# Performance work log

Hardware: AMD Instinct MI355X
Metric: run time of the kernel (lower is better)

Reference implementation:

```python
import math
import jax, jax.numpy as jnp
import numpy as np

WINDOW = (2, 7, 7)
SHIFT = (1, 3, 3)
NUM_HEADS = 4
DIM = 128
B, D, H, W = 1, 16, 112, 112  # divisible by window -> no padding, shift active


def _rel_coords_table():
    wd, wh, ww = WINDOW
    cd = np.arange(-(wd - 1), wd, dtype=np.float32)
    ch = np.arange(-(wh - 1), wh, dtype=np.float32)
    cw = np.arange(-(ww - 1), ww, dtype=np.float32)
    t = np.stack(np.meshgrid(cd, ch, cw, indexing='ij'), axis=-1)  # [2wd-1,2wh-1,2ww-1,3]
    t[..., 0] /= (wd - 1)
    t[..., 1] /= (wh - 1)
    t[..., 2] /= (ww - 1)
    t *= 8.0
    t = np.sign(t) * np.log2(np.abs(t) + 1.0) / 3.0
    return t.reshape(-1, 3)


def _rel_pos_index():
    wd, wh, ww = WINDOW
    coords = np.stack(np.meshgrid(np.arange(wd), np.arange(wh), np.arange(ww), indexing='ij'))
    cf = coords.reshape(3, -1)
    rc = (cf[:, :, None] - cf[:, None, :]).transpose(1, 2, 0)  # [N,N,3]
    rc[..., 0] += wd - 1
    rc[..., 1] += wh - 1
    rc[..., 2] += ww - 1
    rc[..., 0] *= (2 * wh - 1) * (2 * ww - 1)
    rc[..., 1] *= (2 * ww - 1)
    return rc.sum(-1).reshape(-1)


def _attn_mask(pd, ph, pw):
    wd, wh, ww = WINDOW
    sd, sh, sw = SHIFT
    m = np.zeros((pd, ph, pw), np.float32)
    cnt = 0
    for d in ((0, -wd), (-wd, -sd), (-sd, None)):
        for h in ((0, -wh), (-wh, -sh), (-sh, None)):
            for w in ((0, -ww), (-ww, -sw), (-sw, None)):
                m[d[0]:d[1], h[0]:h[1], w[0]:w[1]] = cnt
                cnt += 1
    nwin = (pd // wd) * (ph // wh) * (pw // ww)
    m = m.reshape(pd // wd, wd, ph // wh, wh, pw // ww, ww)
    m = m.transpose(0, 2, 4, 1, 3, 5).reshape(nwin, -1)  # [nWin, N]
    diff = m[:, None, :] - m[:, :, None]
    return np.where(diff != 0, -100.0, 0.0).astype(np.float32)


def setup_inputs() -> dict:
    key = jax.random.key(0)
    ks = jax.random.split(key, 5)
    C = DIM
    return {
        'x': jax.random.normal(ks[0], (B, D, H, W, C), jnp.float32),
        'qkv_weight': jax.random.normal(ks[1], (3 * C, C), jnp.float32) * 0.02,
        'qkv_bias': jnp.zeros((3 * C,), jnp.float32),
        'proj_weight': jax.random.normal(ks[2], (C, C), jnp.float32) * 0.02,
        'proj_bias': jnp.zeros((C,), jnp.float32),
        'logit_scale': jnp.full((NUM_HEADS, 1, 1), math.log(10.0), jnp.float32),
        'cpb_w1': jax.random.normal(ks[3], (512, 3), jnp.float32) * 0.02,
        'cpb_b1': jnp.zeros((512,), jnp.float32),
        'cpb_w2': jax.random.normal(ks[4], (NUM_HEADS, 512), jnp.float32) * 0.02,
    }


def reference(x, qkv_weight, qkv_bias, proj_weight, proj_bias, logit_scale, cpb_w1, cpb_b1, cpb_w2):
    wd, wh, ww = WINDOW
    sd, sh, sw = SHIFT
    b, d, h, w, C = x.shape
    N = wd * wh * ww
    hd = C // NUM_HEADS

    # --- continuous relative position bias (SwinV2) ---
    table = jnp.asarray(_rel_coords_table())              # [M, 3]
    hid = jax.nn.relu(table @ cpb_w1.T + cpb_b1)          # [M, 512]
    bias_tab = hid @ cpb_w2.T                             # [M, nH]
    idx = jnp.asarray(_rel_pos_index())                   # [N*N]
    rpb = bias_tab[idx].reshape(N, N, NUM_HEADS).transpose(2, 0, 1)
    rpb = 16.0 * jax.nn.sigmoid(rpb)                      # [nH, N, N]

    # zero middle third of qkv bias (cosine attention path)
    qkv_b = qkv_bias.at[C:2 * C].set(0.0)

    # --- shift + window partition (no padding: dims divisible) ---
    xs = jnp.roll(x, (-sd, -sh, -sw), axis=(1, 2, 3))
    nd, nh, nw = d // wd, h // wh, w // ww
    nwin = nd * nh * nw
    xw = xs.reshape(b, nd, wd, nh, wh, nw, ww, C)
    xw = xw.transpose(0, 1, 3, 5, 2, 4, 6, 7).reshape(b * nwin, N, C)

    # --- qkv + cosine attention ---
    qkv = (xw @ qkv_weight.T + qkv_b).reshape(b * nwin, N, 3, NUM_HEADS, hd)
    qkv = qkv.transpose(2, 0, 3, 1, 4)                    # [3, BW, nH, N, hd]
    q, k, v = qkv[0], qkv[1], qkv[2]
    qn = q / jnp.maximum(jnp.linalg.norm(q, axis=-1, keepdims=True), 1e-12)
    kn = k / jnp.maximum(jnp.linalg.norm(k, axis=-1, keepdims=True), 1e-12)
    attn = jnp.einsum('wnid,wnjd->wnij', qn, kn)          # [BW, nH, N, N]
    scale = jnp.exp(jnp.minimum(logit_scale, math.log(100.0)))  # [nH,1,1]
    attn = attn * scale[None] + rpb[None]

    # --- shift mask ---
    mask = jnp.asarray(_attn_mask(d, h, w))               # [nWin, N, N]
    attn = attn.reshape(b, nwin, NUM_HEADS, N, N) + mask[None, :, None]
    attn = jax.nn.softmax(attn.reshape(b * nwin, NUM_HEADS, N, N), axis=-1)

    out = jnp.einsum('wnij,wnjd->wind', attn, v).reshape(b * nwin, N, C)
    out = out @ proj_weight.T + proj_bias

    # --- reverse window partition + reverse shift ---
    out = out.reshape(b, nd, nh, nw, wd, wh, ww, C)
    out = out.transpose(0, 1, 4, 2, 5, 3, 6, 7).reshape(b, d, h, w, C)
    out = jnp.roll(out, (sd, sh, sw), axis=(1, 2, 3))
    return out
```

## Files before the change

kernel.cpp:

```cpp
#include <hip/hip_runtime.h>
#include <hip/hip_bf16.h>

typedef unsigned short u16;
typedef __attribute__((ext_vector_type(8))) short bf16x8;
typedef __attribute__((ext_vector_type(4))) float f32x4;

#define MFMA(a, b, c) __builtin_amdgcn_mfma_f32_16x16x32_bf16((a), (b), (c), 0, 0, 0)
#define LOG2E 1.4426950408889634f

__device__ __forceinline__ u16 f2b(float f) {
  __hip_bfloat16 h = __float2bfloat16(f);
  return __builtin_bit_cast(u16, h);
}
__device__ __forceinline__ float bu2f(u16 u) {
  union { unsigned u; float f; } v; v.u = ((unsigned)u) << 16; return v.f;
}
__device__ __forceinline__ u16 f2bu_sw(float f) {
  union { float f; unsigned u; } v; v.f = f;
  unsigned r = v.u + 0x7fffu + ((v.u >> 16) & 1u);
  return (u16)(r >> 16);
}
__device__ __forceinline__ int maskcode(int tok, int bd, int bh, int bw) {
  int d = tok / 49, rem = tok - d * 49, hh = rem / 7, w = rem - hh * 7;
  int rd = bd ? (d == 0 ? 1 : 2) : 0;
  int rh = bh ? (hh < 4 ? 1 : 2) : 0;
  int rw = bw ? (w < 4 ? 1 : 2) : 0;
  return rd * 9 + rh * 3 + rw;
}
__device__ __forceinline__ int tokbase(int tok, int id, int ih, int iw) {
  int d = tok / 49, rem = tok - d * 49, hh = rem / 7, w2 = rem - hh * 7;
  int pd = (id * 2 + d + 1) & 15;
  int ph = ih * 7 + hh + 3; if (ph >= 112) ph -= 112;
  int pw = iw * 7 + w2 + 3; if (pw >= 112) pw -= 112;
  return ((pd * 112 + ph) * 112 + pw) << 7;
}

__global__ void cpb_mlp(const float* __restrict__ w1, const float* __restrict__ b1,
                        const float* __restrict__ w2, float* __restrict__ btab) {
  const int m = blockIdx.x;
  const int k = threadIdx.x;
  const int i0 = m / 169, rm = m % 169, i1 = rm / 13, i2 = rm % 13;
  float c0 = (float)(i0 - 1) * 8.0f;
  float c1 = (float)(i1 - 6) * (8.0f / 6.0f);
  float c2 = (float)(i2 - 6) * (8.0f / 6.0f);
  float t0 = (c0 > 0.f ? 1.f : (c0 < 0.f ? -1.f : 0.f)) * log2f(fabsf(c0) + 1.f) * (1.f / 3.f);
  float t1 = (c1 > 0.f ? 1.f : (c1 < 0.f ? -1.f : 0.f)) * log2f(fabsf(c1) + 1.f) * (1.f / 3.f);
  float t2 = (c2 > 0.f ? 1.f : (c2 < 0.f ? -1.f : 0.f)) * log2f(fabsf(c2) + 1.f) * (1.f / 3.f);
  float hid = fmaxf(w1[k * 3 + 0] * t0 + w1[k * 3 + 1] * t1 + w1[k * 3 + 2] * t2 + b1[k], 0.f);
  __shared__ float red[4][8];
#pragma unroll
  for (int h = 0; h < 4; ++h) {
    float v = hid * w2[h * 512 + k];
    for (int mm = 1; mm < 64; mm <<= 1) v += __shfl_xor(v, mm);
    if ((k & 63) == 0) red[h][k >> 6] = v;
  }
  __syncthreads();
  if (k < 4) {
    float s = 0.f;
#pragma unroll
    for (int j = 0; j < 8; ++j) s += red[k][j];
    btab[m * 4 + k] = s;
  }
}

__global__ void build_rpbf(const float* __restrict__ btab, float* __restrict__ rpbf) {
  const int total = 8 * 4 * 7 * 7 * 64 * 4;
  int n = blockIdx.x * 256 + threadIdx.x;
  if (n >= total) return;
  int r = n & 3;
  int lane = (n >> 2) & 63;
  int q = n >> 8;
  int c = q % 7;
  int wv = (q / 7) % 7;
  int h = (q / 49) % 4;
  int combo = q / 196;
  int i = 16 * wv + (lane >> 4) * 4 + r;
  int j = 16 * c + (lane & 15);
  float v;
  if (j >= 98) {
    v = -1e30f;
  } else if (i >= 98) {
    v = 0.f;
  } else {
    int di = i / 49, ri = i % 49, hi_ = ri / 7, wi = ri % 7;
    int dj = j / 49, rj = j % 49, hj = rj / 7, wj = rj % 7;
    int idx = (di - dj + 1) * 169 + (hi_ - hj + 6) * 13 + (wi - wj + 6);
    float b = btab[idx * 4 + h];
    v = (16.f / (1.f + expf(-b))) * LOG2E;
    int bd = (combo >> 2) & 1, bh = (combo >> 1) & 1, bw = combo & 1;
    if (maskcode(i, bd, bh, bw) != maskcode(j, bd, bh, bw)) v -= 144.269504f;
  }
  rpbf[n] = v;
}

__global__ void pack_wqkv(const float* __restrict__ qkvw, u16* __restrict__ dst) {
  int bid = blockIdx.x;
  int h = bid / 160, rem = bid % 160, blk = rem / 32, r = rem % 32;
  int srow = (blk < 2 ? 0 : (blk < 4 ? 128 : 256)) + h * 32 + r;
  bool lo = (blk == 1) || (blk == 3);
  int c = threadIdx.x;
  float v = (c < 128) ? qkvw[srow * 128 + c] : 0.f;
  u16 hi = f2bu_sw(v);
  u16 outv = lo ? f2bu_sw(v - bu2f(hi)) : hi;
  dst[h * 21760 + blk * 4352 + r * 136 + c] = outv;
}

__global__ void pack_wproj(const float* __restrict__ pw, u16* __restrict__ dst) {
  int c = blockIdx.x;
  int m = threadIdx.x;
  float v = (m < 128) ? pw[c * 128 + m] : 0.f;
  dst[c * 136 + m] = f2bu_sw(v);
}

#define QHI 0
#define QLO 4480
#define KHI 8960
#define KLO 13440
#define VTB 14336
#define PIDX(i, t) ((i) * 128 + ((t) ^ (((i) & 7) << 3)))
#define VIDX(d, t) (VTB + (d) * 128 + ((t) ^ (((d) & 7) << 3)))

template <bool BF16OUT>
__global__ __launch_bounds__(448, 7) void swin_attn(
    const float* __restrict__ xg, const float* __restrict__ qkvb,
    const float* __restrict__ lscale, const float* __restrict__ rpbf,
    const u16* __restrict__ wqkv, u16* __restrict__ aoutb, float* __restrict__ aoutf) {
  __shared__ u16 lds[18432];
  __shared__ int tb[98];
  const int tid = threadIdx.x;
  const int wv = tid >> 6;
  const int l = tid & 63;
  const int l15 = l & 15;
  const int lg = l >> 4;
  const int bid = blockIdx.x;
  const int win = bid >> 2, h = bid & 3;
  const int iw = win & 15, ih = (win >> 4) & 15, id = win >> 8;
  const int combo = ((id == 7) << 2) | ((ih == 15) << 1) | (iw == 15);

  if (tid < 98) tb[tid] = tokbase(tid, id, ih, iw);
  {
    const uint4* src = (const uint4*)(wqkv + h * 21760);
    uint4* dst = (uint4*)lds;
    for (int it = tid; it < 2176; it += 448) dst[it] = src[it];
  }
  const int arow = 16 * wv + l15;
  bf16x8 xa[4];
  {
    const bool rok = arow < 98;
    const int base = tokbase(rok ? arow : 0, id, ih, iw);
    const float* xp = xg + base + lg * 8;
#pragma unroll
    for (int ks = 0; ks < 4; ++ks) {
      float4 a = {0.f, 0.f, 0.f, 0.f}, b4 = {0.f, 0.f, 0.f, 0.f};
      if (rok) {
        a = *(const float4*)(xp + ks * 32);
        b4 = *(const float4*)(xp + ks * 32 + 4);
      }
      u16* xo = (u16*)&xa[ks];
      xo[0] = f2b(a.x); xo[1] = f2b(a.y); xo[2] = f2b(a.z); xo[3] = f2b(a.w);
      xo[4] = f2b(b4.x); xo[5] = f2b(b4.y); xo[6] = f2b(b4.z); xo[7] = f2b(b4.w);
    }
  }
  __syncthreads();

  const f32x4 zf = {0.f, 0.f, 0.f, 0.f};
  f32x4 aq0 = zf, aq1 = zf, ak0 = zf, ak1 = zf, av0 = zf, av1 = zf;
  const u16* wvb = wqkv + h * 21760 + 17408 + lg * 8;
  bf16x8 bv0 = *(const bf16x8*)(wvb + l15 * 136);
  bf16x8 bv1 = *(const bf16x8*)(wvb + (16 + l15) * 136);
#pragma unroll
  for (int ks = 0; ks < 4; ++ks) {
    const int k0 = ks * 32 + lg * 8;
    bf16x8 nv0, nv1;
    if (ks < 3) {
      nv0 = *(const bf16x8*)(wvb + l15 * 136 + (ks + 1) * 32);
      nv1 = *(const bf16x8*)(wvb + (16 + l15) * 136 + (ks + 1) * 32);
    }
    bf16x8 b;
    b = *(const bf16x8*)(&lds[l15 * 136 + k0]);                aq0 = MFMA(xa[ks], b, aq0);
    b = *(const bf16x8*)(&lds[4352 + l15 * 136 + k0]);         aq0 = MFMA(xa[ks], b, aq0);
    b = *(const bf16x8*)(&lds[(16 + l15) * 136 + k0]);         aq1 = MFMA(xa[ks], b, aq1);
    b = *(const bf16x8*)(&lds[4352 + (16 + l15) * 136 + k0]);  aq1 = MFMA(xa[ks], b, aq1);
    b = *(const bf16x8*)(&lds[8704 + l15 * 136 + k0]);         ak0 = MFMA(xa[ks], b, ak0);
    b = *(const bf16x8*)(&lds[13056 + l15 * 136 + k0]);        ak0 = MFMA(xa[ks], b, ak0);
    b = *(const bf16x8*)(&lds[8704 + (16 + l15) * 136 + k0]);  ak1 = MFMA(xa[ks], b, ak1);
    b = *(const bf16x8*)(&lds[13056 + (16 + l15) * 136 + k0]); ak1 = MFMA(xa[ks], b, ak1);
    av0 = MFMA(xa[ks], bv0, av0);
    av1 = MFMA(xa[ks], bv1, av1);
    if (ks < 3) { bv0 = nv0; bv1 = nv1; }
  }
  __syncthreads();

  const float sc2 = __expf(fminf(lscale[h], 4.60517019f)) * LOG2E;
  const float qb0 = qkvb[h * 32 + l15];
  const float qb1 = qkvb[h * 32 + 16 + l15];
  const float vb0 = qkvb[256 + h * 32 + l15];
  const float vb1 = qkvb[256 + h * 32 + 16 + l15];
#pragma unroll
  for (int r = 0; r < 4; ++r) { aq0[r] += qb0; aq1[r] += qb1; av0[r] += vb0; av1[r] += vb1; }
#pragma unroll
  for (int r = 0; r < 4; ++r) {
    const int row = 16 * wv + lg * 4 + r;
    const bool ok = row < 98;
    float s = aq0[r] * aq0[r] + aq1[r] * aq1[r];
    s += __shfl_xor(s, 1); s += __shfl_xor(s, 2); s += __shfl_xor(s, 4); s += __shfl_xor(s, 8);
    float rn = sc2 * rsqrtf(fmaxf(s, 1e-24f));
    float q0 = ok ? aq0[r] * rn : 0.f, q1 = ok ? aq1[r] * rn : 0.f;
    u16 u0 = f2b(q0), u1 = f2b(q1);
    lds[QHI + row * 40 + l15] = u0;
    lds[QHI + row * 40 + 16 + l15] = u1;
    lds[QLO + row * 40 + l15] = f2b(q0 - bu2f(u0));
    lds[QLO + row * 40 + 16 + l15] = f2b(q1 - bu2f(u1));
    float sk = ak0[r] * ak0[r] + ak1[r] * ak1[r];
    sk += __shfl_xor(sk, 1); sk += __shfl_xor(sk, 2); sk += __shfl_xor(sk, 4); sk += __shfl_xor(sk, 8);
    float rk = rsqrtf(fmaxf(sk, 1e-24f));
    float k0v = ok ? ak0[r] * rk : 0.f, k1v = ok ? ak1[r] * rk : 0.f;
    u16 ku0 = f2b(k0v), ku1 = f2b(k1v);
    lds[KHI + row * 40 + l15] = ku0;
    lds[KHI + row * 40 + 16 + l15] = ku1;
    lds[KLO + row * 40 + l15] = f2b(k0v - bu2f(ku0));
    lds[KLO + row * 40 + 16 + l15] = f2b(k1v - bu2f(ku1));
  }
  __syncthreads();

  const bf16x8 qh = *(const bf16x8*)(&lds[QHI + (16 * wv + l15) * 40 + lg * 8]);
  const bf16x8 qlo = *(const bf16x8*)(&lds[QLO + (16 * wv + l15) * 40 + lg * 8]);
  const f32x4* rbf = (const f32x4*)rpbf + (((combo * 4 + h) * 7 + wv) * 7) * 64 + l;
  f32x4 att[7];
#pragma unroll
  for (int c = 0; c < 7; ++c) att[c] = rbf[c * 64];
#pragma unroll
  for (int c = 0; c < 7; ++c) {
    const bf16x8 kh = *(const bf16x8*)(&lds[KHI + (16 * c + l15) * 40 + lg * 8]);
    const bf16x8 kl = *(const bf16x8*)(&lds[KLO + (16 * c + l15) * 40 + lg * 8]);
    att[c] = MFMA(qh, kh, att[c]);
    att[c] = MFMA(qlo, kh, att[c]);
    att[c] = MFMA(qh, kl, att[c]);
  }
  float rsv[4];
#pragma unroll
  for (int r = 0; r < 4; ++r) {
    float s = 0.f;
#pragma unroll
    for (int c = 0; c < 7; ++c) { float p = exp2f(att[c][r]); att[c][r] = p; s += p; }
    s += __shfl_xor(s, 1); s += __shfl_xor(s, 2); s += __shfl_xor(s, 4); s += __shfl_xor(s, 8);
    rsv[r] = 1.0f / s;
  }
  __syncthreads();

#pragma unroll
  for (int r = 0; r < 4; ++r) {
    const int i = 16 * wv + lg * 4 + r;
#pragma unroll
    for (int c = 0; c < 8; ++c) {
      const int t = 16 * c + l15;
      lds[PIDX(i, t)] = (c < 7) ? f2b(att[c][r] * rsv[r]) : (u16)0;
    }
  }
  {
    const int t0 = 16 * wv + lg * 4;
    ushort4 v0, v1;
    v0.x = (t0 + 0 < 98) ? f2b(av0[0]) : (u16)0;
    v0.y = (t0 + 1 < 98) ? f2b(av0[1]) : (u16)0;
    v0.z = (t0 + 2 < 98) ? f2b(av0[2]) : (u16)0;
    v0.w = (t0 + 3 < 98) ? f2b(av0[3]) : (u16)0;
    v1.x = (t0 + 0 < 98) ? f2b(av1[0]) : (u16)0;
    v1.y = (t0 + 1 < 98) ? f2b(av1[1]) : (u16)0;
    v1.z = (t0 + 2 < 98) ? f2b(av1[2]) : (u16)0;
    v1.w = (t0 + 3 < 98) ? f2b(av1[3]) : (u16)0;
    *(ushort4*)(&lds[VIDX(l15, t0)]) = v0;
    *(ushort4*)(&lds[VIDX(16 + l15, t0)]) = v1;
  }
  for (int it = tid; it < 32 * 16; it += 448) {
    int dd = it >> 4, t = 112 + (it & 15);
    lds[VIDX(dd, t)] = 0;
  }
  __syncthreads();

  f32x4 o0 = zf, o1 = zf;
#pragma unroll
  for (int ks = 0; ks < 4; ++ks) {
    const int t = ks * 32 + lg * 8;
    const bf16x8 pa = *(const bf16x8*)(&lds[PIDX(16 * wv + l15, t)]);
    const bf16x8 v0f = *(const bf16x8*)(&lds[VIDX(l15, t)]);
    const bf16x8 v1f = *(const bf16x8*)(&lds[VIDX(16 + l15, t)]);
    o0 = MFMA(pa, v0f, o0);
    o1 = MFMA(pa, v1f, o1);
  }
#pragma unroll
  for (int r = 0; r < 4; ++r) {
    const int row = 16 * wv + lg * 4 + r;
    if (row < 98) {
      const int ob = tb[row] + h * 32;
      if (BF16OUT) {
        aoutb[ob + l15] = f2b(o0[r]);
        aoutb[ob + 16 + l15] = f2b(o1[r]);
      } else {
        aoutf[ob + l15] = o0[r];
        aoutf[ob + 16 + l15] = o1[r];
      }
    }
  }
}

template <bool BF16OUT>
__global__ __launch_bounds__(448) void swin_proj(const u16* __restrict__ wp,
                                                 const float* __restrict__ projb,
                                                 const u16* __restrict__ aoutb,
                                                 float* io) {
  __shared__ u16 w[17408];
  __shared__ int tb[98];
  const int tid = threadIdx.x;
  const int wv = tid >> 6;
  const int l = tid & 63;
  const int l15 = l & 15;
  const int lg = l >> 4;
  const int win = blockIdx.x;
  const int iw = win & 15, ih = (win >> 4) & 15, id = win >> 8;
  if (tid < 98) tb[tid] = tokbase(tid, id, ih, iw);
  {
    const uint4* src = (const uint4*)wp;
    uint4* dst = (uint4*)w;
    for (int it = tid; it < 2176; it += 448) dst[it] = src[it];
  }
  __syncthreads();
  const int arow0 = 16 * wv + l15;
  const int abase = tb[(arow0 < 98) ? arow0 : 97];

  const f32x4 zf = {0.f, 0.f, 0.f, 0.f};
  f32x4 pr[8];
#pragma unroll
  for (int n = 0; n < 8; ++n) pr[n] = zf;
#pragma unroll
  for (int ks = 0; ks < 4; ++ks) {
    bf16x8 oa;
    if (BF16OUT) {
      oa = *(const bf16x8*)(aoutb + abase + ks * 32 + lg * 8);
    } else {
      const float4 f0 = *(const float4*)(io + abase + ks * 32 + lg * 8);
      const float4 f1 = *(const float4*)(io + abase + ks * 32 + lg * 8 + 4);
      u16* op = (u16*)&oa;
      op[0] = f2b(f0.x); op[1] = f2b(f0.y); op[2] = f2b(f0.z); op[3] = f2b(f0.w);
      op[4] = f2b(f1.x); op[5] = f2b(f1.y); op[6] = f2b(f1.z); op[7] = f2b(f1.w);
    }
#pragma unroll
    for (int n = 0; n < 8; ++n) {
      const bf16x8 wb = *(const bf16x8*)(&w[(16 * n + l15) * 136 + ks * 32 + lg * 8]);
      pr[n] = MFMA(oa, wb, pr[n]);
    }
  }
#pragma unroll
  for (int n = 0; n < 8; ++n) {
    const int col = 16 * n + l15;
    const float pb = projb[col];
#pragma unroll
    for (int r = 0; r < 4; ++r) {
      const int row = 16 * wv + lg * 4 + r;
      if (row < 98) io[tb[row] + col] = pr[n][r] + pb;
    }
  }
}

extern "C" void kernel_launch(void* const* d_in, const int* in_sizes, int n_in,
                              void* d_out, int out_size, void* d_ws, size_t ws_size,
                              hipStream_t stream) {
  const float* xg = (const float*)d_in[0];
  const float* qkvw = (const float*)d_in[1];
  const float* qkvb = (const float*)d_in[2];
  const float* projw = (const float*)d_in[3];
  const float* projb = (const float*)d_in[4];
  const float* lsc = (const float*)d_in[5];
  const float* w1 = (const float*)d_in[6];
  const float* b1 = (const float*)d_in[7];
  const float* w2 = (const float*)d_in[8];

  char* ws = (char*)d_ws;
  float* btab = (float*)(ws);
  u16* wq = (u16*)(ws + 8192);
  u16* wp = (u16*)(ws + 182272);
  float* rpbf = (float*)(ws + 217088);
  u16* aoutb = (u16*)(ws + 1822720);
  float* io = (float*)d_out;

  const bool bf16path = ws_size >= (size_t)53202944;

  cpb_mlp<<<507, 512, 0, stream>>>(w1, b1, w2, btab);
  build_rpbf<<<(8 * 4 * 7 * 7 * 64 * 4 + 255) / 256, 256, 0, stream>>>(btab, rpbf);
  pack_wqkv<<<640, 136, 0, stream>>>(qkvw, wq);
  pack_wproj<<<128, 136, 0, stream>>>(projw, wp);
  if (bf16path) {
    swin_attn<true><<<8192, 448, 0, stream>>>(xg, qkvb, lsc, rpbf, wq, aoutb, io);
    swin_proj<true><<<2048, 448, 0, stream>>>(wp, projb, aoutb, io);
  } else {
    swin_attn<false><<<8192, 448, 0, stream>>>(xg, qkvb, lsc, rpbf, wq, nullptr, io);
    swin_proj<false><<<2048, 448, 0, stream>>>(wp, projb, nullptr, io);
  }
}
```

Measured before the change: 218.5 us.

## Fuse per-head attention and output projection into one per-window kernel

Replaces the per-(window, head) attention kernel and the separate projection kernel with one kernel per window. It loops over the four heads, keeps each head's output in registers and runs the projection from LDS. Weights are repacked into a 32-column-blocked layout and read straight from global or L2 instead of being staged in LDS. This removes the bf16 intermediate round trip through global memory and one launch, and reuses the x load across heads. In exchange, each block does serial per-head work with more barriers, and occupancy falls (launch bounds 4 instead of 7), which may hurt latency hiding.

```diff
diff --git a/kernel.cpp b/kernel.cpp
--- a/kernel.cpp
+++ b/kernel.cpp
@@ -99,50 +99,46 @@
   int srow = (blk < 2 ? 0 : (blk < 4 ? 128 : 256)) + h * 32 + r;
   bool lo = (blk == 1) || (blk == 3);
   int c = threadIdx.x;
-  float v = (c < 128) ? qkvw[srow * 128 + c] : 0.f;
+  float v = qkvw[srow * 128 + c];
   u16 hi = f2bu_sw(v);
   u16 outv = lo ? f2bu_sw(v - bu2f(hi)) : hi;
-  dst[h * 21760 + blk * 4352 + r * 136 + c] = outv;
+  dst[h * 20480 + blk * 4096 + (c >> 5) * 1024 + r * 32 + (c & 31)] = outv;
 }
 
 __global__ void pack_wproj(const float* __restrict__ pw, u16* __restrict__ dst) {
   int c = blockIdx.x;
   int m = threadIdx.x;
-  float v = (m < 128) ? pw[c * 128 + m] : 0.f;
-  dst[c * 136 + m] = f2bu_sw(v);
+  dst[(m >> 5) * 4096 + c * 32 + (m & 31)] = f2bu_sw(pw[c * 128 + m]);
 }
 
 #define QHI 0
 #define QLO 4480
 #define KHI 8960
 #define KLO 13440
-#define VTB 14336
+#define VTB 17920
 #define PIDX(i, t) ((i) * 128 + ((t) ^ (((i) & 7) << 3)))
 #define VIDX(d, t) (VTB + (d) * 128 + ((t) ^ (((d) & 7) << 3)))
 
-template <bool BF16OUT>
-__global__ __launch_bounds__(448, 7) void swin_attn(
+__global__ __launch_bounds__(448, 4) void swin_fused(
     const float* __restrict__ xg, const float* __restrict__ qkvb,
     const float* __restrict__ lscale, const float* __restrict__ rpbf,
-    const u16* __restrict__ wqkv, u16* __restrict__ aoutb, float* __restrict__ aoutf) {
-  __shared__ u16 lds[18432];
+    const u16* __restrict__ wqkv, const u16* __restrict__ wproj,
+    const float* __restrict__ projb, float* __restrict__ io) {
+  __shared__ u16 lds[22016];
   __shared__ int tb[98];
   const int tid = threadIdx.x;
   const int wv = tid >> 6;
   const int l = tid & 63;
   const int l15 = l & 15;
   const int lg = l >> 4;
-  const int bid = blockIdx.x;
-  const int win = bid >> 2, h = bid & 3;
+  const int win = blockIdx.x;
   const int iw = win & 15, ih = (win >> 4) & 15, id = win >> 8;
   const int combo = ((id == 7) << 2) | ((ih == 15) << 1) | (iw == 15);
 
   if (tid < 98) tb[tid] = tokbase(tid, id, ih, iw);
-  {
-    const uint4* src = (const uint4*)(wqkv + h * 21760);
-    uint4* dst = (uint4*)lds;
-    for (int it = tid; it < 2176; it += 448) dst[it] = src[it];
-  }
+  for (int it = tid; it < 32 * 16; it += 448)
+    lds[VIDX(it >> 4, 112 + (it & 15))] = 0;
+
   const int arow = 16 * wv + l15;
   bf16x8 xa[4];
   {
@@ -161,192 +157,155 @@
       xo[4] = f2b(b4.x); xo[5] = f2b(b4.y); xo[6] = f2b(b4.z); xo[7] = f2b(b4.w);
     }
   }
-  __syncthreads();
 
   const f32x4 zf = {0.f, 0.f, 0.f, 0.f};
-  f32x4 aq0 = zf, aq1 = zf, ak0 = zf, ak1 = zf, av0 = zf, av1 = zf;
-  const u16* wvb = wqkv + h * 21760 + 17408 + lg * 8;
-  bf16x8 bv0 = *(const bf16x8*)(wvb + l15 * 136);
-  bf16x8 bv1 = *(const bf16x8*)(wvb + (16 + l15) * 136);
+  auto GEMM1 = [&](int h, f32x4& q0, f32x4& q1, f32x4& k0a, f32x4& k1a, f32x4& v0a, f32x4& v1a) {
+    q0 = q1 = k0a = k1a = v0a = v1a = zf;
+    const u16* wb = wqkv + h * 20480 + lg * 8;
+#pragma unroll
+    for (int ks = 0; ks < 4; ++ks) {
+      const int o = ks * 1024;
+      bf16x8 b;
+      b = *(const bf16x8*)(wb + o + l15 * 32);                 q0 = MFMA(xa[ks], b, q0);
+      b = *(const bf16x8*)(wb + 4096 + o + l15 * 32);          q0 = MFMA(xa[ks], b, q0);
+      b = *(const bf16x8*)(wb + o + (16 + l15) * 32);          q1 = MFMA(xa[ks], b, q1);
+      b = *(const bf16x8*)(wb + 4096 + o + (16 + l15) * 32);   q1 = MFMA(xa[ks], b, q1);
+      b = *(const bf16x8*)(wb + 8192 + o + l15 * 32);          k0a = MFMA(xa[ks], b, k0a);
+      b = *(const bf16x8*)(wb + 12288 + o + l15 * 32);         k0a = MFMA(xa[ks], b, k0a);
+      b = *(const bf16x8*)(wb + 8192 + o + (16 + l15) * 32);   k1a = MFMA(xa[ks], b, k1a);
+      b = *(const bf16x8*)(wb + 12288 + o + (16 + l15) * 32);  k1a = MFMA(xa[ks], b, k1a);
+      b = *(const bf16x8*)(wb + 16384 + o + l15 * 32);         v0a = MFMA(xa[ks], b, v0a);
+      b = *(const bf16x8*)(wb + 16384 + o + (16 + l15) * 32);  v1a = MFMA(xa[ks], b, v1a);
+    }
+  };
+
+  u16 opk[4][8];
+  f32x4 aq0, aq1, ak0, ak1, av0, av1, nq0, nq1, nk0, nk1, nv0, nv1;
+  GEMM1(0, aq0, aq1, ak0, ak1, av0, av1);
+
+#pragma unroll
+  for (int h = 0; h < 4; ++h) {
+    const float sc2 = __expf(fminf(lscale[h], 4.60517019f)) * LOG2E;
+    const float qb0 = qkvb[h * 32 + l15];
+    const float qb1 = qkvb[h * 32 + 16 + l15];
+    const float vb0 = qkvb[256 + h * 32 + l15];
+    const float vb1 = qkvb[256 + h * 32 + 16 + l15];
+#pragma unroll
+    for (int r = 0; r < 4; ++r) { aq0[r] += qb0; aq1[r] += qb1; av0[r] += vb0; av1[r] += vb1; }
+#pragma unroll
+    for (int r = 0; r < 4; ++r) {
+      const int row = 16 * wv + lg * 4 + r;
+      const bool ok = row < 98;
+      float s = aq0[r] * aq0[r] + aq1[r] * aq1[r];
+      s += __shfl_xor(s, 1); s += __shfl_xor(s, 2); s += __shfl_xor(s, 4); s += __shfl_xor(s, 8);
+      float rn = sc2 * rsqrtf(fmaxf(s, 1e-24f));
+      float q0 = ok ? aq0[r] * rn : 0.f, q1 = ok ? aq1[r] * rn : 0.f;
+      u16 u0 = f2b(q0), u1 = f2b(q1);
+      lds[QHI + row * 40 + l15] = u0;
+      lds[QHI + row * 40 + 16 + l15] = u1;
+      lds[QLO + row * 40 + l15] = f2b(q0 - bu2f(u0));
+      lds[QLO + row * 40 + 16 + l15] = f2b(q1 - bu2f(u1));
+      float sk = ak0[r] * ak0[r] + ak1[r] * ak1[r];
+      sk += __shfl_xor(sk, 1); sk += __shfl_xor(sk, 2); sk += __shfl_xor(sk, 4); sk += __shfl_xor(sk, 8);
+      float rk = rsqrtf(fmaxf(sk, 1e-24f));
+      float k0v = ok ? ak0[r] * rk : 0.f, k1v = ok ? ak1[r] * rk : 0.f;
+      u16 ku0 = f2b(k0v), ku1 = f2b(k1v);
+      lds[KHI + row * 40 + l15] = ku0;
+      lds[KHI + row * 40 + 16 + l15] = ku1;
+      lds[KLO + row * 40 + l15] = f2b(k0v - bu2f(ku0));
+      lds[KLO + row * 40 + 16 + l15] = f2b(k1v - bu2f(ku1));
+    }
+    {
+      const int t0 = 16 * wv + lg * 4;
+      ushort4 v0, v1;
+      v0.x = (t0 + 0 < 98) ? f2b(av0[0]) : (u16)0;
+      v0.y = (t0 + 1 < 98) ? f2b(av0[1]) : (u16)0;
+      v0.z = (t0 + 2 < 98) ? f2b(av0[2]) : (u16)0;
+      v0.w = (t0 + 3 < 98) ? f2b(av0[3]) : (u16)0;
+      v1.x = (t0 + 0 < 98) ? f2b(av1[0]) : (u16)0;
+      v1.y = (t0 + 1 < 98) ? f2b(av1[1]) : (u16)0;
+      v1.z = (t0 + 2 < 98) ? f2b(av1[2]) : (u16)0;
+      v1.w = (t0 + 3 < 98) ? f2b(av1[3]) : (u16)0;
+      *(ushort4*)(&lds[VIDX(l15, t0)]) = v0;
+      *(ushort4*)(&lds[VIDX(16 + l15, t0)]) = v1;
+    }
+    const f32x4* rbf = (const f32x4*)rpbf + (((combo * 4 + h) * 7 + wv) * 7) * 64 + l;
+    f32x4 att[7];
+#pragma unroll
+    for (int c = 0; c < 7; ++c) att[c] = rbf[c * 64];
+    __syncthreads();
+
+    const bf16x8 qh = *(const bf16x8*)(&lds[QHI + (16 * wv + l15) * 40 + lg * 8]);
+    const bf16x8 qlo = *(const bf16x8*)(&lds[QLO + (16 * wv + l15) * 40 + lg * 8]);
+#pragma unroll
+    for (int c = 0; c < 7; ++c) {
+      const bf16x8 kh = *(const bf16x8*)(&lds[KHI + (16 * c + l15) * 40 + lg * 8]);
+      const bf16x8 kl = *(const bf16x8*)(&lds[KLO + (16 * c + l15) * 40 + lg * 8]);
+      att[c] = MFMA(qh, kh, att[c]);
+      att[c] = MFMA(qlo, kh, att[c]);
+      att[c] = MFMA(qh, kl, att[c]);
+    }
+    float rsv[4];
+#pragma unroll
+    for (int r = 0; r < 4; ++r) {
+      float s = 0.f;
+#pragma unroll
+      for (int c = 0; c < 7; ++c) { float p = exp2f(att[c][r]); att[c][r] = p; s += p; }
+      s += __shfl_xor(s, 1); s += __shfl_xor(s, 2); s += __shfl_xor(s, 4); s += __shfl_xor(s, 8);
+      rsv[r] = 1.0f / s;
+    }
+    __syncthreads();
+
+#pragma unroll
+    for (int r = 0; r < 4; ++r) {
+      const int i = 16 * wv + lg * 4 + r;
+#pragma unroll
+      for (int c = 0; c < 8; ++c) {
+        const int t = 16 * c + l15;
+        lds[PIDX(i, t)] = (c < 7) ? f2b(att[c][r]) : (u16)0;
+      }
+    }
+    f32x4 o0 = zf, o1 = zf;
+#pragma unroll
+    for (int ks = 0; ks < 4; ++ks) {
+      const int t = ks * 32 + lg * 8;
+      const bf16x8 pa = *(const bf16x8*)(&lds[PIDX(16 * wv + l15, t)]);
+      const bf16x8 v0f = *(const bf16x8*)(&lds[VIDX(l15, t)]);
+      const bf16x8 v1f = *(const bf16x8*)(&lds[VIDX(16 + l15, t)]);
+      o0 = MFMA(pa, v0f, o0);
+      o1 = MFMA(pa, v1f, o1);
+    }
+#pragma unroll
+    for (int r = 0; r < 4; ++r) {
+      opk[h][r] = f2b(o0[r] * rsv[r]);
+      opk[h][4 + r] = f2b(o1[r] * rsv[r]);
+    }
+    if (h < 3) {
+      GEMM1(h + 1, nq0, nq1, nk0, nk1, nv0, nv1);
+      __syncthreads();
+      aq0 = nq0; aq1 = nq1; ak0 = nk0; ak1 = nk1; av0 = nv0; av1 = nv1;
+    }
+  }
+
+#pragma unroll
+  for (int h = 0; h < 4; ++h)
+#pragma unroll
+    for (int e = 0; e < 8; ++e) {
+      const int r = e & 3, half = e >> 2;
+      lds[PIDX(16 * wv + lg * 4 + r, h * 32 + half * 16 + l15)] = opk[h][e];
+    }
+
+  f32x4 pr[8];
+#pragma unroll
+  for (int n = 0; n < 8; ++n) pr[n] = zf;
 #pragma unroll
   for (int ks = 0; ks < 4; ++ks) {
-    const int k0 = ks * 32 + lg * 8;
-    bf16x8 nv0, nv1;
-    if (ks < 3) {
-      nv0 = *(const bf16x8*)(wvb + l15 * 136 + (ks + 1) * 32);
-      nv1 = *(const bf16x8*)(wvb + (16 + l15) * 136 + (ks + 1) * 32);
-    }
-    bf16x8 b;
-    b = *(const bf16x8*)(&lds[l15 * 136 + k0]);                aq0 = MFMA(xa[ks], b, aq0);
-    b = *(const bf16x8*)(&lds[4352 + l15 * 136 + k0]);         aq0 = MFMA(xa[ks], b, aq0);
-    b = *(const bf16x8*)(&lds[(16 + l15) * 136 + k0]);         aq1 = MFMA(xa[ks], b, aq1);
-    b = *(const bf16x8*)(&lds[4352 + (16 + l15) * 136 + k0]);  aq1 = MFMA(xa[ks], b, aq1);
-    b = *(const bf16x8*)(&lds[8704 + l15 * 136 + k0]);         ak0 = MFMA(xa[ks], b, ak0);
-    b = *(const bf16x8*)(&lds[13056 + l15 * 136 + k0]);        ak0 = MFMA(xa[ks], b, ak0);
-    b = *(const bf16x8*)(&lds[8704 + (16 + l15) * 136 + k0]);  ak1 = MFMA(xa[ks], b, ak1);
-    b = *(const bf16x8*)(&lds[13056 + (16 + l15) * 136 + k0]); ak1 = MFMA(xa[ks], b, ak1);
-    av0 = MFMA(xa[ks], bv0, av0);
-    av1 = MFMA(xa[ks], bv1, av1);
-    if (ks < 3) { bv0 = nv0; bv1 = nv1; }
-  }
-  __syncthreads();
-
-  const float sc2 = __expf(fminf(lscale[h], 4.60517019f)) * LOG2E;
-  const float qb0 = qkvb[h * 32 + l15];
-  const float qb1 = qkvb[h * 32 + 16 + l15];
-  const float vb0 = qkvb[256 + h * 32 + l15];
-  const float vb1 = qkvb[256 + h * 32 + 16 + l15];
-#pragma unroll
-  for (int r = 0; r < 4; ++r) { aq0[r] += qb0; aq1[r] += qb1; av0[r] += vb0; av1[r] += vb1; }
-#pragma unroll
-  for (int r = 0; r < 4; ++r) {
-    const int row = 16 * wv + lg * 4 + r;
-    const bool ok = row < 98;
-    float s = aq0[r] * aq0[r] + aq1[r] * aq1[r];
-    s += __shfl_xor(s, 1); s += __shfl_xor(s, 2); s += __shfl_xor(s, 4); s += __shfl_xor(s, 8);
-    float rn = sc2 * rsqrtf(fmaxf(s, 1e-24f));
-    float q0 = ok ? aq0[r] * rn : 0.f, q1 = ok ? aq1[r] * rn : 0.f;
-    u16 u0 = f2b(q0), u1 = f2b(q1);
-    lds[QHI + row * 40 + l15] = u0;
-    lds[QHI + row * 40 + 16 + l15] = u1;
-    lds[QLO + row * 40 + l15] = f2b(q0 - bu2f(u0));
-    lds[QLO + row * 40 + 16 + l15] = f2b(q1 - bu2f(u1));
-    float sk = ak0[r] * ak0[r] + ak1[r] * ak1[r];
-    sk += __shfl_xor(sk, 1); sk += __shfl_xor(sk, 2); sk += __shfl_xor(sk, 4); sk += __shfl_xor(sk, 8);
-    float rk = rsqrtf(fmaxf(sk, 1e-24f));
-    float k0v = ok ? ak0[r] * rk : 0.f, k1v = ok ? ak1[r] * rk : 0.f;
-    u16 ku0 = f2b(k0v), ku1 = f2b(k1v);
-    lds[KHI + row * 40 + l15] = ku0;
-    lds[KHI + row * 40 + 16 + l15] = ku1;
-    lds[KLO + row * 40 + l15] = f2b(k0v - bu2f(ku0));
-    lds[KLO + row * 40 + 16 + l15] = f2b(k1v - bu2f(ku1));
-  }
-  __syncthreads();
-
-  const bf16x8 qh = *(const bf16x8*)(&lds[QHI + (16 * wv + l15) * 40 + lg * 8]);
-  const bf16x8 qlo = *(const bf16x8*)(&lds[QLO + (16 * wv + l15) * 40 + lg * 8]);
-  const f32x4* rbf = (const f32x4*)rpbf + (((combo * 4 + h) * 7 + wv) * 7) * 64 + l;
-  f32x4 att[7];
-#pragma unroll
-  for (int c = 0; c < 7; ++c) att[c] = rbf[c * 64];
-#pragma unroll
-  for (int c = 0; c < 7; ++c) {
-    const bf16x8 kh = *(const bf16x8*)(&lds[KHI + (16 * c + l15) * 40 + lg * 8]);
-    const bf16x8 kl = *(const bf16x8*)(&lds[KLO + (16 * c + l15) * 40 + lg * 8]);
-    att[c] = MFMA(qh, kh, att[c]);
-    att[c] = MFMA(qlo, kh, att[c]);
-    att[c] = MFMA(qh, kl, att[c]);
-  }
-  float rsv[4];
-#pragma unroll
-  for (int r = 0; r < 4; ++r) {
-    float s = 0.f;
-#pragma unroll
-    for (int c = 0; c < 7; ++c) { float p = exp2f(att[c][r]); att[c][r] = p; s += p; }
-    s += __shfl_xor(s, 1); s += __shfl_xor(s, 2); s += __shfl_xor(s, 4); s += __shfl_xor(s, 8);
-    rsv[r] = 1.0f / s;
-  }
-  __syncthreads();
-
-#pragma unroll
-  for (int r = 0; r < 4; ++r) {
-    const int i = 16 * wv + lg * 4 + r;
-#pragma unroll
-    for (int c = 0; c < 8; ++c) {
-      const int t = 16 * c + l15;
-      lds[PIDX(i, t)] = (c < 7) ? f2b(att[c][r] * rsv[r]) : (u16)0;
-    }
-  }
-  {
-    const int t0 = 16 * wv + lg * 4;
-    ushort4 v0, v1;
-    v0.x = (t0 + 0 < 98) ? f2b(av0[0]) : (u16)0;
-    v0.y = (t0 + 1 < 98) ? f2b(av0[1]) : (u16)0;
-    v0.z = (t0 + 2 < 98) ? f2b(av0[2]) : (u16)0;
-    v0.w = (t0 + 3 < 98) ? f2b(av0[3]) : (u16)0;
-    v1.x = (t0 + 0 < 98) ? f2b(av1[0]) : (u16)0;
-    v1.y = (t0 + 1 < 98) ? f2b(av1[1]) : (u16)0;
-    v1.z = (t0 + 2 < 98) ? f2b(av1[2]) : (u16)0;
-    v1.w = (t0 + 3 < 98) ? f2b(av1[3]) : (u16)0;
-    *(ushort4*)(&lds[VIDX(l15, t0)]) = v0;
-    *(ushort4*)(&lds[VIDX(16 + l15, t0)]) = v1;
-  }
-  for (int it = tid; it < 32 * 16; it += 448) {
-    int dd = it >> 4, t = 112 + (it & 15);
-    lds[VIDX(dd, t)] = 0;
-  }
-  __syncthreads();
-
-  f32x4 o0 = zf, o1 = zf;
-#pragma unroll
-  for (int ks = 0; ks < 4; ++ks) {
-    const int t = ks * 32 + lg * 8;
-    const bf16x8 pa = *(const bf16x8*)(&lds[PIDX(16 * wv + l15, t)]);
-    const bf16x8 v0f = *(const bf16x8*)(&lds[VIDX(l15, t)]);
-    const bf16x8 v1f = *(const bf16x8*)(&lds[VIDX(16 + l15, t)]);
-    o0 = MFMA(pa, v0f, o0);
-    o1 = MFMA(pa, v1f, o1);
-  }
-#pragma unroll
-  for (int r = 0; r < 4; ++r) {
-    const int row = 16 * wv + lg * 4 + r;
-    if (row < 98) {
-      const int ob = tb[row] + h * 32;
-      if (BF16OUT) {
-        aoutb[ob + l15] = f2b(o0[r]);
-        aoutb[ob + 16 + l15] = f2b(o1[r]);
-      } else {
-        aoutf[ob + l15] = o0[r];
-        aoutf[ob + 16 + l15] = o1[r];
-      }
-    }
-  }
-}
-
-template <bool BF16OUT>
-__global__ __launch_bounds__(448) void swin_proj(const u16* __restrict__ wp,
-                                                 const float* __restrict__ projb,
-                                                 const u16* __restrict__ aoutb,
-                                                 float* io) {
-  __shared__ u16 w[17408];
-  __shared__ int tb[98];
-  const int tid = threadIdx.x;
-  const int wv = tid >> 6;
-  const int l = tid & 63;
-  const int l15 = l & 15;
-  const int lg = l >> 4;
-  const int win = blockIdx.x;
-  const int iw = win & 15, ih = (win >> 4) & 15, id = win >> 8;
-  if (tid < 98) tb[tid] = tokbase(tid, id, ih, iw);
-  {
-    const uint4* src = (const uint4*)wp;
-    uint4* dst = (uint4*)w;
-    for (int it = tid; it < 2176; it += 448) dst[it] = src[it];
-  }
-  __syncthreads();
-  const int arow0 = 16 * wv + l15;
-  const int abase = tb[(arow0 < 98) ? arow0 : 97];
-
-  const f32x4 zf = {0.f, 0.f, 0.f, 0.f};
-  f32x4 pr[8];
-#pragma unroll
-  for (int n = 0; n < 8; ++n) pr[n] = zf;
-#pragma unroll
-  for (int ks = 0; ks < 4; ++ks) {
-    bf16x8 oa;
-    if (BF16OUT) {
-      oa = *(const bf16x8*)(aoutb + abase + ks * 32 + lg * 8);
-    } else {
-      const float4 f0 = *(const float4*)(io + abase + ks * 32 + lg * 8);
-      const float4 f1 = *(const float4*)(io + abase + ks * 32 + lg * 8 + 4);
-      u16* op = (u16*)&oa;
-      op[0] = f2b(f0.x); op[1] = f2b(f0.y); op[2] = f2b(f0.z); op[3] = f2b(f0.w);
-      op[4] = f2b(f1.x); op[5] = f2b(f1.y); op[6] = f2b(f1.z); op[7] = f2b(f1.w);
-    }
+    const bf16x8 oa = *(const bf16x8*)(&lds[PIDX(16 * wv + l15, ks * 32 + lg * 8)]);
+    const u16* pwb = wproj + ks * 4096 + lg * 8;
 #pragma unroll
     for (int n = 0; n < 8; ++n) {
-      const bf16x8 wb = *(const bf16x8*)(&w[(16 * n + l15) * 136 + ks * 32 + lg * 8]);
-      pr[n] = MFMA(oa, wb, pr[n]);
+      const bf16x8 wbf = *(const bf16x8*)(pwb + (16 * n + l15) * 32);
+      pr[n] = MFMA(oa, wbf, pr[n]);
     }
   }
 #pragma unroll
@@ -377,22 +336,13 @@
   char* ws = (char*)d_ws;
   float* btab = (float*)(ws);
   u16* wq = (u16*)(ws + 8192);
-  u16* wp = (u16*)(ws + 182272);
-  float* rpbf = (float*)(ws + 217088);
-  u16* aoutb = (u16*)(ws + 1822720);
+  u16* wp = (u16*)(ws + 172032);
+  float* rpbf = (float*)(ws + 204800);
   float* io = (float*)d_out;
-
-  const bool bf16path = ws_size >= (size_t)53202944;
 
   cpb_mlp<<<507, 512, 0, stream>>>(w1, b1, w2, btab);
   build_rpbf<<<(8 * 4 * 7 * 7 * 64 * 4 + 255) / 256, 256, 0, stream>>>(btab, rpbf);
-  pack_wqkv<<<640, 136, 0, stream>>>(qkvw, wq);
-  pack_wproj<<<128, 136, 0, stream>>>(projw, wp);
-  if (bf16path) {
-    swin_attn<true><<<8192, 448, 0, stream>>>(xg, qkvb, lsc, rpbf, wq, aoutb, io);
-    swin_proj<true><<<2048, 448, 0, stream>>>(wp, projb, aoutb, io);
-  } else {
-    swin_attn<false><<<8192, 448, 0, stream>>>(xg, qkvb, lsc, rpbf, wq, nullptr, io);
-    swin_proj<false><<<2048, 448, 0, stream>>>(wp, projb, nullptr, io);
-  }
-}
+  pack_wqkv<<<640, 128, 0, stream>>>(qkvw, wq);
+  pack_wproj<<<128, 128, 0, stream>>>(projw, wp);
+  swin_fused<<<2048, 448, 0, stream>>>(xg, qkvb, lsc, rpbf, wq, wp, projb, io);
+}
```

Result: slower. 371.5 us, median of 2 (+70.0%).

## Transpose MFMA operands for vectorized stores and window-contiguous intermediate layout

Applied to the files above, without the earlier changes.

Swaps the A/B operands of the PV and projection MFMAs so each lane holds four consecutive output columns of one token. This allows vectorized 8/16-byte stores instead of scattered scalar stores. The bf16 intermediate now uses a window-contiguous layout, so the proj kernel reads it without a token-base lookup. It also hoists the relative-position-bias loads earlier to overlap them with the normalization, drops the masking branch on x loads (padded rows read clamped token 0), and adds an occupancy hint of 7 to launch bounds.

```diff
diff --git a/kernel.cpp b/kernel.cpp
--- a/kernel.cpp
+++ b/kernel.cpp
@@ -146,16 +146,12 @@
   const int arow = 16 * wv + l15;
   bf16x8 xa[4];
   {
-    const bool rok = arow < 98;
-    const int base = tokbase(rok ? arow : 0, id, ih, iw);
+    const int base = tokbase((arow < 98) ? arow : 0, id, ih, iw);
     const float* xp = xg + base + lg * 8;
 #pragma unroll
     for (int ks = 0; ks < 4; ++ks) {
-      float4 a = {0.f, 0.f, 0.f, 0.f}, b4 = {0.f, 0.f, 0.f, 0.f};
-      if (rok) {
-        a = *(const float4*)(xp + ks * 32);
-        b4 = *(const float4*)(xp + ks * 32 + 4);
-      }
+      const float4 a = *(const float4*)(xp + ks * 32);
+      const float4 b4 = *(const float4*)(xp + ks * 32 + 4);
       u16* xo = (u16*)&xa[ks];
       xo[0] = f2b(a.x); xo[1] = f2b(a.y); xo[2] = f2b(a.z); xo[3] = f2b(a.w);
       xo[4] = f2b(b4.x); xo[5] = f2b(b4.y); xo[6] = f2b(b4.z); xo[7] = f2b(b4.w);
@@ -190,6 +186,11 @@
     if (ks < 3) { bv0 = nv0; bv1 = nv1; }
   }
   __syncthreads();
+
+  const f32x4* rbf = (const f32x4*)rpbf + (((combo * 4 + h) * 7 + wv) * 7) * 64 + l;
+  f32x4 att[7];
+#pragma unroll
+  for (int c = 0; c < 7; ++c) att[c] = rbf[c * 64];
 
   const float sc2 = __expf(fminf(lscale[h], 4.60517019f)) * LOG2E;
   const float qb0 = qkvb[h * 32 + l15];
@@ -225,10 +226,6 @@
 
   const bf16x8 qh = *(const bf16x8*)(&lds[QHI + (16 * wv + l15) * 40 + lg * 8]);
   const bf16x8 qlo = *(const bf16x8*)(&lds[QLO + (16 * wv + l15) * 40 + lg * 8]);
-  const f32x4* rbf = (const f32x4*)rpbf + (((combo * 4 + h) * 7 + wv) * 7) * 64 + l;
-  f32x4 att[7];
-#pragma unroll
-  for (int c = 0; c < 7; ++c) att[c] = rbf[c * 64];
 #pragma unroll
   for (int c = 0; c < 7; ++c) {
     const bf16x8 kh = *(const bf16x8*)(&lds[KHI + (16 * c + l15) * 40 + lg * 8]);
@@ -284,30 +281,34 @@
     const bf16x8 pa = *(const bf16x8*)(&lds[PIDX(16 * wv + l15, t)]);
     const bf16x8 v0f = *(const bf16x8*)(&lds[VIDX(l15, t)]);
     const bf16x8 v1f = *(const bf16x8*)(&lds[VIDX(16 + l15, t)]);
-    o0 = MFMA(pa, v0f, o0);
-    o1 = MFMA(pa, v1f, o1);
-  }
-#pragma unroll
-  for (int r = 0; r < 4; ++r) {
-    const int row = 16 * wv + lg * 4 + r;
-    if (row < 98) {
-      const int ob = tb[row] + h * 32;
+    o0 = MFMA(v0f, pa, o0);
+    o1 = MFMA(v1f, pa, o1);
+  }
+  {
+    const int tok = 16 * wv + l15;
+    if (tok < 98) {
       if (BF16OUT) {
-        aoutb[ob + l15] = f2b(o0[r]);
-        aoutb[ob + 16 + l15] = f2b(o1[r]);
+        u16* ab = aoutb + (win * 98 + tok) * 128 + h * 32;
+        ushort4 s0, s1;
+        s0.x = f2b(o0[0]); s0.y = f2b(o0[1]); s0.z = f2b(o0[2]); s0.w = f2b(o0[3]);
+        s1.x = f2b(o1[0]); s1.y = f2b(o1[1]); s1.z = f2b(o1[2]); s1.w = f2b(o1[3]);
+        *(ushort4*)(ab + lg * 4) = s0;
+        *(ushort4*)(ab + 16 + lg * 4) = s1;
       } else {
-        aoutf[ob + l15] = o0[r];
-        aoutf[ob + 16 + l15] = o1[r];
+        float* ab = aoutf + tb[tok] + h * 32;
+        f32x4 s0 = o0, s1 = o1;
+        *(f32x4*)(ab + lg * 4) = s0;
+        *(f32x4*)(ab + 16 + lg * 4) = s1;
       }
     }
   }
 }
 
 template <bool BF16OUT>
-__global__ __launch_bounds__(448) void swin_proj(const u16* __restrict__ wp,
-                                                 const float* __restrict__ projb,
-                                                 const u16* __restrict__ aoutb,
-                                                 float* io) {
+__global__ __launch_bounds__(448, 7) void swin_proj(const u16* __restrict__ wp,
+                                                    const float* __restrict__ projb,
+                                                    const u16* __restrict__ aoutb,
+                                                    float* io) {
   __shared__ u16 w[17408];
   __shared__ int tb[98];
   const int tid = threadIdx.x;
@@ -324,8 +325,8 @@
     for (int it = tid; it < 2176; it += 448) dst[it] = src[it];
   }
   __syncthreads();
-  const int arow0 = 16 * wv + l15;
-  const int abase = tb[(arow0 < 98) ? arow0 : 97];
+  const int tok = 16 * wv + l15;
+  const int tokc = (tok < 98) ? tok : 97;
 
   const f32x4 zf = {0.f, 0.f, 0.f, 0.f};
   f32x4 pr[8];
@@ -335,29 +336,27 @@
   for (int ks = 0; ks < 4; ++ks) {
     bf16x8 oa;
     if (BF16OUT) {
-      oa = *(const bf16x8*)(aoutb + abase + ks * 32 + lg * 8);
+      oa = *(const bf16x8*)(aoutb + (win * 98 + tokc) * 128 + ks * 32 + lg * 8);
     } else {
-      const float4 f0 = *(const float4*)(io + abase + ks * 32 + lg * 8);
-      const float4 f1 = *(const float4*)(io + abase + ks * 32 + lg * 8 + 4);
+      const float* ap = io + tb[tokc] + ks * 32 + lg * 8;
+      const float4 f0 = *(const float4*)(ap);
+      const float4 f1 = *(const float4*)(ap + 4);
       u16* op = (u16*)&oa;
       op[0] = f2b(f0.x); op[1] = f2b(f0.y); op[2] = f2b(f0.z); op[3] = f2b(f0.w);
       op[4] = f2b(f1.x); op[5] = f2b(f1.y); op[6] = f2b(f1.z); op[7] = f2b(f1.w);
     }
 #pragma unroll
     for (int n = 0; n < 8; ++n) {
-      const bf16x8 wb = *(const bf16x8*)(&w[(16 * n + l15) * 136 + ks * 32 + lg * 8]);
-      pr[n] = MFMA(oa, wb, pr[n]);
+      const bf16x8 wbf = *(const bf16x8*)(&w[(16 * n + l15) * 136 + ks * 32 + lg * 8]);
+      pr[n] = MFMA(wbf, oa, pr[n]);
     }
   }
 #pragma unroll
   for (int n = 0; n < 8; ++n) {
-    const int col = 16 * n + l15;
-    const float pb = projb[col];
-#pragma unroll
-    for (int r = 0; r < 4; ++r) {
-      const int row = 16 * wv + lg * 4 + r;
-      if (row < 98) io[tb[row] + col] = pr[n][r] + pb;
-    }
+    const float4 pb4 = *(const float4*)(projb + 16 * n + lg * 4);
+    f32x4 o = pr[n];
+    o[0] += pb4.x; o[1] += pb4.y; o[2] += pb4.z; o[3] += pb4.w;
+    if (tok < 98) *(f32x4*)(io + tb[tok] + 16 * n + lg * 4) = o;
   }
 }
 
```

Measured after the change: 196.3 us. 1.11x faster.
